# Kernel tuning notes

Measured on AMD Instinct MI355X. Metric: run time of the kernel, lower is better.

The kernel has to match this reference:

```python
import jax, jax.numpy as jnp
import numpy as np

B, H, S, D = 4, 16, 2048, 64
SCALE = 8.0  # sqrt(D)
NEG = -1000000000.0


def setup_inputs() -> dict:
    key = jax.random.key(0)
    kq, kk, kv = jax.random.split(key, 3)
    q = jax.random.normal(kq, (B, H, S, D), dtype=jnp.float32)
    k = jax.random.normal(kk, (B, H, S, D), dtype=jnp.float32)
    v = jax.random.normal(kv, (B, H, S, D), dtype=jnp.float32)
    # causal mask: True means masked out (matches torch masked_fill)
    mask = jnp.triu(jnp.ones((S, S), dtype=bool), k=1)[None, None, :, :]
    mask = jnp.broadcast_to(mask, (B, 1, S, S))
    return {"q": q, "k": k, "v": v, "mask": mask}


def reference(q, k, v, mask):
    # score = q @ k^T / scale  -> [B,H,S,S]
    score = jnp.einsum("bhqd,bhkd->bhqk", q, k) / SCALE
    score = jnp.where(mask, NEG, score)
    probs = jax.nn.softmax(score, axis=-1)
    context = jnp.einsum("bhqk,bhkd->bhqd", probs, v)
    return context
```

## Files before the change

kernel.cpp:

```cpp
#include <hip/hip_runtime.h>

#define SQ 2048
#define DH 64
#define BK 64
#define NQT 32
#define NBH 64
#define M0 8.0f

#define WS_BYTES ((size_t)2 * NBH * SQ * DH * 2)

typedef float f32x4 __attribute__((ext_vector_type(4)));
typedef __bf16 bf16x8 __attribute__((ext_vector_type(8)));
typedef _Float16 f16x4 __attribute__((ext_vector_type(4)));
typedef _Float16 f16x8 __attribute__((ext_vector_type(8)));
typedef __fp16 fp16x2 __attribute__((ext_vector_type(2)));
typedef unsigned short u16x8 __attribute__((ext_vector_type(8)));
typedef unsigned int u32x4 __attribute__((ext_vector_type(4)));

static __device__ __forceinline__ unsigned int pkbf(float a, float b) {
#if __has_builtin(__builtin_amdgcn_cvt_pk_bf16_f32)
  typedef __bf16 bf16x2 __attribute__((ext_vector_type(2)));
  bf16x2 r = __builtin_amdgcn_cvt_pk_bf16_f32(a, b);
  return __builtin_bit_cast(unsigned int, r);
#else
  unsigned int ua = __builtin_bit_cast(unsigned int, a);
  unsigned int ub = __builtin_bit_cast(unsigned int, b);
  ua += 0x7fffu + ((ua >> 16) & 1u);
  ub += 0x7fffu + ((ub >> 16) & 1u);
  return (ua >> 16) | (ub & 0xffff0000u);
#endif
}

static __device__ __forceinline__ unsigned int pkf16(float a, float b) {
  fp16x2 r = __builtin_amdgcn_cvt_pkrtz(a, b);
  return __builtin_bit_cast(unsigned int, r);
}

static __device__ __forceinline__ f32x4 mfma_qk(u16x8 a, u16x8 b, f32x4 c) {
  return __builtin_amdgcn_mfma_f32_16x16x32_bf16(
      __builtin_bit_cast(bf16x8, a), __builtin_bit_cast(bf16x8, b), c, 0, 0, 0);
}

static __device__ __forceinline__ f32x4 mfma_pv(f16x4 a, f16x4 b, f32x4 c) {
  return __builtin_amdgcn_mfma_f32_16x16x16f16(a, b, c, 0, 0, 0);
}

static __device__ __forceinline__ f32x4 mfma_pv32(f16x8 a, f16x8 b, f32x4 c) {
  return __builtin_amdgcn_mfma_f32_16x16x32_f16(a, b, c, 0, 0, 0);
}

static __device__ __forceinline__ void ld16(unsigned short* l, const unsigned short* g) {
  __builtin_amdgcn_global_load_lds(
      (const __attribute__((address_space(1))) unsigned int*)(const void*)g,
      (__attribute__((address_space(3))) unsigned int*)(void*)l, 16, 0, 0);
}

static __device__ __forceinline__ void store_tile(float* wb, float* dst,
                                                  const f32x4* o, int lane,
                                                  int l15, int quad) {
#pragma unroll
  for (int dt = 0; dt < 4; ++dt) {
    const int colw = dt * 16 + quad * 4;
    *(f32x4*)&wb[l15 * 64 + (colw ^ ((l15 & 3) * 16))] = o[dt];
  }
  __builtin_amdgcn_wave_barrier();
#pragma unroll
  for (int j = 0; j < 4; ++j) {
    const int row = j * 4 + (lane >> 4);
    const int colw = (lane & 15) * 4;
    f32x4 v = *(const f32x4*)&wb[row * 64 + (colw ^ ((row & 3) * 16))];
    *(f32x4*)&dst[row * 64 + colw] = v;
  }
}

__global__ __launch_bounds__(256) void prep(const float* __restrict__ K,
                                            const float* __restrict__ V,
                                            unsigned short* __restrict__ Kf,
                                            unsigned short* __restrict__ Vf) {
  const int bh = (int)blockIdx.x >> 5;
  const int st = (int)blockIdx.x & 31;
  const int tid = threadIdx.x;
  __shared__ __align__(16) unsigned short T[DH * 64];
  {
    const int kvb = (tid >> 4) * 4, vdb = (tid & 15) * 4;
    const float* vp = V + ((size_t)bh * SQ + st * 64 + kvb) * DH + vdb;
    f32x4 r0 = *(const f32x4*)vp, r1 = *(const f32x4*)(vp + DH),
          r2 = *(const f32x4*)(vp + 2 * DH), r3 = *(const f32x4*)(vp + 3 * DH);
    const int uu = kvb >> 3, h = (kvb >> 2) & 1;
#pragma unroll
    for (int i = 0; i < 4; ++i) {
      const int d = vdb + i;
      uint2 w = {pkf16(r0[i], r1[i]), pkf16(r2[i], r3[i])};
      *(uint2*)&T[d * 64 + ((uu ^ (d & 7)) * 8) + h * 4] = w;
    }
  }
  {
    const size_t kin = ((size_t)bh * SQ + st * 64) * DH;
    unsigned short* kfo = Kf + (size_t)bh * SQ * DH + (size_t)st * 64 * DH;
#pragma unroll
    for (int e = 0; e < 2; ++e) {
      const int L = tid * 2 + e;
      const int l15 = L & 15, quad = (L >> 4) & 3, c = (L >> 6) & 1, nt = (L >> 7) & 3;
      const int krow = (nt >> 1) * 32 + ((l15 >> 2) & 3) * 8 + (nt & 1) * 4 + (l15 & 3);
      const float* kp = K + kin + (size_t)krow * DH + (c * 4 + quad) * 8;
      f32x4 x = *(const f32x4*)kp, y = *(const f32x4*)(kp + 4);
      u32x4 w = {pkbf(x[0], x[1]), pkbf(x[2], x[3]), pkbf(y[0], y[1]), pkbf(y[2], y[3])};
      *(u32x4*)&kfo[L * 8] = w;
    }
  }
  __syncthreads();
  {
    unsigned short* vfo = Vf + (size_t)bh * SQ * DH + (size_t)st * 64 * DH;
#pragma unroll
    for (int e = 0; e < 2; ++e) {
      const int L = tid * 2 + e;
      const int l15 = L & 15, quad = (L >> 4) & 3, dt = (L >> 6) & 3, n2 = (L >> 8) & 1;
      const int d = dt * 16 + l15, uu = n2 * 4 + quad;
      u16x8 val = *(const u16x8*)&T[d * 64 + ((uu ^ (d & 7)) * 8)];
      *(u16x8*)&vfo[L * 8] = val;
    }
  }
}

__global__ __launch_bounds__(256, 4) void fa_main(
    const float* __restrict__ Q, const unsigned short* __restrict__ Kf,
    const unsigned short* __restrict__ Vf, float* __restrict__ O) {
  const int lin = (int)blockIdx.x;
  const int xcd = lin & 7, u = lin >> 3;
  const int hh = u & 7;
  const int pi = (int)((0x32104567BA98CDEFull >> ((u >> 3) * 4)) & 15u);
  const int bh = hh * 8 + xcd;
  const int tend = 2 * pi + 1;

  const int tid = threadIdx.x;
  const int wv = tid >> 6;
  const int lane = tid & 63;
  const int l15 = lane & 15;
  const int quad = lane >> 4;

  __shared__ __align__(16) unsigned short SS[2][BK * DH];

  const size_t hq = (size_t)bh * (SQ * DH);
  const unsigned short* KfH = Kf + (size_t)bh * SQ * DH;
  const unsigned short* VfH = Vf + (size_t)bh * SQ * DH;

  const int qbase = pi * 128 + wv * 32;
  const int dtw = 2 * pi + (wv >> 1);
  const int qo = (wv & 1) * 32;

  u16x8 qf[2][2];
  {
    const float scq = 0.125f * 1.4426950408889634f;
#pragma unroll
    for (int f = 0; f < 2; ++f) {
      const float* qp = Q + hq + (size_t)(qbase + 16 * f + l15) * DH + quad * 8;
#pragma unroll
      for (int c = 0; c < 2; ++c) {
        f32x4 x = *(const f32x4*)(qp + c * 32);
        f32x4 y = *(const f32x4*)(qp + c * 32 + 4);
        u32x4 w = {pkbf(x[0] * scq, x[1] * scq), pkbf(x[2] * scq, x[3] * scq),
                   pkbf(y[0] * scq, y[1] * scq), pkbf(y[2] * scq, y[3] * scq)};
        qf[f][c] = __builtin_bit_cast(u16x8, w);
      }
    }
  }

  f32x4 o0[4], o1[4], la0, la1;
#pragma unroll
  for (int dt = 0; dt < 4; ++dt) {
    o0[dt] = (f32x4){0.f, 0.f, 0.f, 0.f};
    o1[dt] = (f32x4){0.f, 0.f, 0.f, 0.f};
  }
  la0 = (f32x4){0.f, 0.f, 0.f, 0.f};
  la1 = (f32x4){0.f, 0.f, 0.f, 0.f};
  const f16x8 ones8 = {(_Float16)1.f, (_Float16)1.f, (_Float16)1.f, (_Float16)1.f,
                       (_Float16)1.f, (_Float16)1.f, (_Float16)1.f, (_Float16)1.f};

  auto stage = [&](unsigned short* W, int t) {
#pragma unroll
    for (int j = 0; j < 2; ++j) {
      const int off = wv * 1024 + j * 512 + lane * 8;
      ld16(&W[off], &KfH[(size_t)t * 4096 + off]);
    }
  };

  auto attend = [&](const unsigned short* Ks, int t, bool diag) {
    const unsigned short* vg = VfH + (size_t)t * 4096;
    f16x8 vb0[4];
#pragma unroll
    for (int dt = 0; dt < 4; ++dt)
      vb0[dt] = *(const f16x8*)&vg[(0 * 4 + dt) * 512 + lane * 8];
    f32x4 s0[4], s1[4];
#pragma unroll
    for (int nt = 0; nt < 4; ++nt) {
      f32x4 a0 = {-M0, -M0, -M0, -M0}, a1 = {-M0, -M0, -M0, -M0};
#pragma unroll
      for (int c = 0; c < 2; ++c) {
        u16x8 kf = *(const u16x8*)&Ks[(nt * 2 + c) * 512 + lane * 8];
        a0 = mfma_qk(kf, qf[0][c], a0);
        a1 = mfma_qk(kf, qf[1][c], a1);
      }
      s0[nt] = a0;
      s1[nt] = a1;
    }
    if (diag) {
#pragma unroll
      for (int nt = 0; nt < 4; ++nt)
#pragma unroll
        for (int r = 0; r < 4; ++r) {
          const int kvl = (nt >> 1) * 32 + quad * 8 + (nt & 1) * 4 + r;
          if (kvl > qo + l15) s0[nt][r] = -1e30f;
          if (kvl > qo + 16 + l15) s1[nt][r] = -1e30f;
        }
    }
    f16x8 pf0[2], pf1[2];
#pragma unroll
    for (int n2 = 0; n2 < 2; ++n2) {
      f32x4 pe0, po0, pe1, po1;
#pragma unroll
      for (int r = 0; r < 4; ++r) {
        pe0[r] = __builtin_amdgcn_exp2f(s0[2 * n2][r]);
        po0[r] = __builtin_amdgcn_exp2f(s0[2 * n2 + 1][r]);
        pe1[r] = __builtin_amdgcn_exp2f(s1[2 * n2][r]);
        po1[r] = __builtin_amdgcn_exp2f(s1[2 * n2 + 1][r]);
      }
      u32x4 w0 = {pkf16(pe0[0], pe0[1]), pkf16(pe0[2], pe0[3]),
                  pkf16(po0[0], po0[1]), pkf16(po0[2], po0[3])};
      u32x4 w1 = {pkf16(pe1[0], pe1[1]), pkf16(pe1[2], pe1[3]),
                  pkf16(po1[0], po1[1]), pkf16(po1[2], po1[3])};
      pf0[n2] = __builtin_bit_cast(f16x8, w0);
      pf1[n2] = __builtin_bit_cast(f16x8, w1);
    }
    f16x8 vb1[4];
#pragma unroll
    for (int dt = 0; dt < 4; ++dt)
      vb1[dt] = *(const f16x8*)&vg[(1 * 4 + dt) * 512 + lane * 8];
    la0 = mfma_pv32(ones8, pf0[0], la0);
    la1 = mfma_pv32(ones8, pf1[0], la1);
    la0 = mfma_pv32(ones8, pf0[1], la0);
    la1 = mfma_pv32(ones8, pf1[1], la1);
#pragma unroll
    for (int dt = 0; dt < 4; ++dt) {
      o0[dt] = mfma_pv32(vb0[dt], pf0[0], o0[dt]);
      o1[dt] = mfma_pv32(vb0[dt], pf1[0], o1[dt]);
    }
#pragma unroll
    for (int dt = 0; dt < 4; ++dt) {
      o0[dt] = mfma_pv32(vb1[dt], pf0[1], o0[dt]);
      o1[dt] = mfma_pv32(vb1[dt], pf1[1], o1[dt]);
    }
  };

  auto step = [&](int t, const unsigned short* R, unsigned short* W) {
    if (t <= dtw) attend(R, t, t == dtw);
    __syncthreads();
    if (t + 2 <= tend) stage(W, t + 2);
  };

  stage(SS[0], 0);
  __syncthreads();
  stage(SS[1], 1);
  for (int t = 0; t <= tend; t += 2) {
    step(t, SS[0], SS[0]);
    if (t + 1 <= tend) step(t + 1, SS[1], SS[1]);
  }

  float* wb = (float*)SS + wv * 1024;
  {
    const float inv = 1.0f / la0[0];
    f32x4 on[4];
#pragma unroll
    for (int dt = 0; dt < 4; ++dt) on[dt] = o0[dt] * inv;
    store_tile(wb, O + hq + (size_t)(qbase)*DH, on, lane, l15, quad);
  }
  {
    const float inv = 1.0f / la1[0];
    f32x4 on[4];
#pragma unroll
    for (int dt = 0; dt < 4; ++dt) on[dt] = o1[dt] * inv;
    store_tile(wb, O + hq + (size_t)(qbase + 16) * DH, on, lane, l15, quad);
  }
}

__global__ __launch_bounds__(256, 4) void fa_full(
    const float* __restrict__ Q, const float* __restrict__ K,
    const float* __restrict__ V, float* __restrict__ O) {
  const int lin = (int)blockIdx.x;
  const int xcd = lin & 7;
  const int u = lin >> 3;
  const int hh = u & 7;
  const int p = u >> 3;
  const int bh = hh * 8 + xcd;
  const int tid = threadIdx.x;
  const int wv = tid >> 6;
  const int lane = tid & 63;
  const int l15 = lane & 15;
  const int quad = lane >> 4;
  __shared__ __align__(16) unsigned short SMEM[2][2 * BK * DH];
  const size_t hbase = (size_t)bh * (SQ * DH);
  const int krr = tid >> 3, kcc = (tid & 7) * 8;
  const int kvb = (tid >> 4) * 4, vdb = (tid & 15) * 4;
#pragma unroll
  for (int ph = 0; ph < 2; ++ph) {
    const int qt = ph ? (NQT - 1 - p) : p;
    const int wq0 = qt * 64 + wv * 16;
    u16x8 qf[2];
    {
      const float scq = 0.125f * 1.4426950408889634f;
      const float* qp = Q + hbase + (size_t)(wq0 + l15) * DH + quad * 8;
#pragma unroll
      for (int c = 0; c < 2; ++c) {
        f32x4 x = *(const f32x4*)(qp + c * 32);
        f32x4 y = *(const f32x4*)(qp + c * 32 + 4);
        u32x4 w = {pkbf(x[0] * scq, x[1] * scq), pkbf(x[2] * scq, x[3] * scq),
                   pkbf(y[0] * scq, y[1] * scq), pkbf(y[2] * scq, y[3] * scq)};
        qf[c] = __builtin_bit_cast(u16x8, w);
      }
    }
    f32x4 o[4];
#pragma unroll
    for (int dt = 0; dt < 4; ++dt) o[dt] = (f32x4){0.f, 0.f, 0.f, 0.f};
    float l = 0.f;
    f32x4 ka[2][2], va[4];
    {
      const float* kp = K + hbase + (size_t)krr * DH + kcc;
      ka[0][0] = *(const f32x4*)kp;             ka[0][1] = *(const f32x4*)(kp + 4);
      ka[1][0] = *(const f32x4*)(kp + 32 * DH); ka[1][1] = *(const f32x4*)(kp + 32 * DH + 4);
      const float* vp = V + hbase + (size_t)kvb * DH + vdb;
      va[0] = *(const f32x4*)vp;            va[1] = *(const f32x4*)(vp + DH);
      va[2] = *(const f32x4*)(vp + 2 * DH); va[3] = *(const f32x4*)(vp + 3 * DH);
    }
    __syncthreads();
    {
      unsigned short* Ksn = SMEM[0];
      unsigned short* Vsn = SMEM[0] + BK * DH;
#pragma unroll
      for (int h = 0; h < 2; ++h) {
        const int rr = h * 32 + krr;
        u32x4 w = {pkbf(ka[h][0][0], ka[h][0][1]), pkbf(ka[h][0][2], ka[h][0][3]),
                   pkbf(ka[h][1][0], ka[h][1][1]), pkbf(ka[h][1][2], ka[h][1][3])};
        *(u32x4*)&Ksn[rr * DH + (kcc ^ ((rr & 7) * 8))] = w;
      }
#pragma unroll
      for (int i = 0; i < 4; ++i) {
        const int d = vdb + i;
        uint2 w = {pkf16(va[0][i], va[1][i]), pkf16(va[2][i], va[3][i])};
        *(uint2*)&Vsn[d * BK + (kvb ^ ((d & 15) * 4))] = w;
      }
    }
    __syncthreads();
    for (int t = 0; t <= qt; ++t) {
      const unsigned short* Ks = SMEM[t & 1];
      const unsigned short* Vs = SMEM[t & 1] + BK * DH;
      if (t < qt) {
        const int kb2 = (t + 1) * BK;
        const float* kp = K + hbase + (size_t)(kb2 + krr) * DH + kcc;
        ka[0][0] = *(const f32x4*)kp;             ka[0][1] = *(const f32x4*)(kp + 4);
        ka[1][0] = *(const f32x4*)(kp + 32 * DH); ka[1][1] = *(const f32x4*)(kp + 32 * DH + 4);
        const float* vp = V + hbase + (size_t)(kb2 + kvb) * DH + vdb;
        va[0] = *(const f32x4*)vp;            va[1] = *(const f32x4*)(vp + DH);
        va[2] = *(const f32x4*)(vp + 2 * DH); va[3] = *(const f32x4*)(vp + 3 * DH);
      }
      f32x4 s[4];
#pragma unroll
      for (int nt = 0; nt < 4; ++nt) {
        f32x4 acc = {-M0, -M0, -M0, -M0};
#pragma unroll
        for (int c = 0; c < 2; ++c) {
          const int row = nt * 16 + l15;
          u16x8 kf = *(const u16x8*)&Ks[row * DH + ((c * 32 + quad * 8) ^ ((l15 & 7) * 8))];
          acc = mfma_qk(kf, qf[c], acc);
        }
        s[nt] = acc;
      }
      if (t == qt) {
#pragma unroll
        for (int nt = 0; nt < 4; ++nt)
#pragma unroll
          for (int r = 0; r < 4; ++r)
            if (nt * 16 + quad * 4 + r > wv * 16 + l15) s[nt][r] = -1e30f;
      }
      f16x4 pf[4];
#pragma unroll
      for (int nt = 0; nt < 4; ++nt) {
        f32x4 pr;
#pragma unroll
        for (int r = 0; r < 4; ++r) { pr[r] = __builtin_amdgcn_exp2f(s[nt][r]); l += pr[r]; }
        uint2 w2 = {pkf16(pr[0], pr[1]), pkf16(pr[2], pr[3])};
        pf[nt] = __builtin_bit_cast(f16x4, w2);
      }
#pragma unroll
      for (int dt = 0; dt < 4; ++dt) {
        const int d = dt * 16 + l15;
#pragma unroll
        for (int nt = 0; nt < 4; ++nt) {
          f16x4 vf = *(const f16x4*)&Vs[d * BK + ((nt * 16 + quad * 4) ^ (l15 * 4))];
          o[dt] = mfma_pv(vf, pf[nt], o[dt]);
        }
      }
      if (t < qt) {
        unsigned short* Ksn = SMEM[(t + 1) & 1];
        unsigned short* Vsn = SMEM[(t + 1) & 1] + BK * DH;
#pragma unroll
        for (int h = 0; h < 2; ++h) {
          const int rr = h * 32 + krr;
          u32x4 w = {pkbf(ka[h][0][0], ka[h][0][1]), pkbf(ka[h][0][2], ka[h][0][3]),
                     pkbf(ka[h][1][0], ka[h][1][1]), pkbf(ka[h][1][2], ka[h][1][3])};
          *(u32x4*)&Ksn[rr * DH + (kcc ^ ((rr & 7) * 8))] = w;
        }
#pragma unroll
        for (int i = 0; i < 4; ++i) {
          const int d = vdb + i;
          uint2 w = {pkf16(va[0][i], va[1][i]), pkf16(va[2][i], va[3][i])};
          *(uint2*)&Vsn[d * BK + (kvb ^ ((d & 15) * 4))] = w;
        }
        __syncthreads();
      }
    }
    l += __shfl_xor(l, 16, 64);
    l += __shfl_xor(l, 32, 64);
    const float inv = 1.0f / l;
    f32x4 on[4];
#pragma unroll
    for (int dt = 0; dt < 4; ++dt) on[dt] = o[dt] * inv;
    float* wb = (float*)SMEM[(qt + 1) & 1] + wv * 1024;
    store_tile(wb, O + hbase + (size_t)wq0 * DH, on, lane, l15, quad);
  }
}

extern "C" void kernel_launch(void* const* d_in, const int* in_sizes, int n_in,
                              void* d_out, int out_size, void* d_ws, size_t ws_size,
                              hipStream_t stream) {
  const float* q = (const float*)d_in[0];
  const float* k = (const float*)d_in[1];
  const float* v = (const float*)d_in[2];
  float* o = (float*)d_out;
  if (ws_size >= WS_BYTES) {
    unsigned short* Kf = (unsigned short*)d_ws;
    unsigned short* Vf = Kf + (size_t)NBH * SQ * DH;
    prep<<<dim3(NBH * 32), 256, 0, stream>>>(k, v, Kf, Vf);
    fa_main<<<dim3(1024), 256, 0, stream>>>(q, Kf, Vf, o);
  } else {
    fa_full<<<dim3(1024), 256, 0, stream>>>(q, k, v, o);
  }
}
```

Before: 206.9 us.

## Stage K and V through a 4-deep LDS ring with 512-thread blocks

Doubles the block to 8 waves covering 256 query rows, so the grid drops to 512 blocks and each K/V tile is shared by more waves. K and V tiles are now both staged into LDS with async loads in a 4-slot ring buffer, three tiles ahead. Manual vmcnt waits and raw barriers replace __syncthreads. The aim is to hide global latency and cut redundant V reads from global memory. In exchange it uses far more LDS per block, which may limit occupancy, and the hand-tuned wait counts are fragile.

After: 204.0 us. No clear change (-1.4%).

```diff
diff --git a/kernel.cpp b/kernel.cpp
--- a/kernel.cpp
+++ b/kernel.cpp
@@ -16,6 +16,8 @@
 typedef __fp16 fp16x2 __attribute__((ext_vector_type(2)));
 typedef unsigned short u16x8 __attribute__((ext_vector_type(8)));
 typedef unsigned int u32x4 __attribute__((ext_vector_type(4)));
+
+#define WAIT_VM(N) asm volatile("s_waitcnt vmcnt(" #N ")" ::: "memory")
 
 static __device__ __forceinline__ unsigned int pkbf(float a, float b) {
 #if __has_builtin(__builtin_amdgcn_cvt_pk_bf16_f32)
@@ -122,15 +124,15 @@
   }
 }
 
-__global__ __launch_bounds__(256, 4) void fa_main(
+__global__ __launch_bounds__(512, 4) void fa_main(
     const float* __restrict__ Q, const unsigned short* __restrict__ Kf,
     const unsigned short* __restrict__ Vf, float* __restrict__ O) {
   const int lin = (int)blockIdx.x;
   const int xcd = lin & 7, u = lin >> 3;
   const int hh = u & 7;
-  const int pi = (int)((0x32104567BA98CDEFull >> ((u >> 3) * 4)) & 15u);
+  const int p = (int)((0x32104567u >> ((u >> 3) * 4)) & 15u);
   const int bh = hh * 8 + xcd;
-  const int tend = 2 * pi + 1;
+  const int tend = 4 * p + 3;
 
   const int tid = threadIdx.x;
   const int wv = tid >> 6;
@@ -138,14 +140,14 @@
   const int l15 = lane & 15;
   const int quad = lane >> 4;
 
-  __shared__ __align__(16) unsigned short SS[2][BK * DH];
+  __shared__ __align__(16) unsigned short SS[4][8192];
 
   const size_t hq = (size_t)bh * (SQ * DH);
   const unsigned short* KfH = Kf + (size_t)bh * SQ * DH;
   const unsigned short* VfH = Vf + (size_t)bh * SQ * DH;
 
-  const int qbase = pi * 128 + wv * 32;
-  const int dtw = 2 * pi + (wv >> 1);
+  const int qbase = p * 256 + wv * 32;
+  const int dtw = 4 * p + (wv >> 1);
   const int qo = (wv & 1) * 32;
 
   u16x8 qf[2][2];
@@ -180,16 +182,16 @@
 #pragma unroll
     for (int j = 0; j < 2; ++j) {
       const int off = wv * 1024 + j * 512 + lane * 8;
-      ld16(&W[off], &KfH[(size_t)t * 4096 + off]);
+      const unsigned short* src = (off < 4096)
+                                      ? &KfH[(size_t)t * 4096 + off]
+                                      : &VfH[(size_t)t * 4096 + (off - 4096)];
+      ld16(&W[off], src);
     }
   };
 
-  auto attend = [&](const unsigned short* Ks, int t, bool diag) {
-    const unsigned short* vg = VfH + (size_t)t * 4096;
-    f16x8 vb0[4];
-#pragma unroll
-    for (int dt = 0; dt < 4; ++dt)
-      vb0[dt] = *(const f16x8*)&vg[(0 * 4 + dt) * 512 + lane * 8];
+  auto attend = [&](const unsigned short* B, bool diag) {
+    const unsigned short* Ks = B;
+    const unsigned short* Vs = B + 4096;
     f32x4 s0[4], s1[4];
 #pragma unroll
     for (int nt = 0; nt < 4; ++nt) {
@@ -231,38 +233,42 @@
       pf0[n2] = __builtin_bit_cast(f16x8, w0);
       pf1[n2] = __builtin_bit_cast(f16x8, w1);
     }
-    f16x8 vb1[4];
-#pragma unroll
-    for (int dt = 0; dt < 4; ++dt)
-      vb1[dt] = *(const f16x8*)&vg[(1 * 4 + dt) * 512 + lane * 8];
-    la0 = mfma_pv32(ones8, pf0[0], la0);
-    la1 = mfma_pv32(ones8, pf1[0], la1);
-    la0 = mfma_pv32(ones8, pf0[1], la0);
-    la1 = mfma_pv32(ones8, pf1[1], la1);
+#pragma unroll
+    for (int n2 = 0; n2 < 2; ++n2) {
+      la0 = mfma_pv32(ones8, pf0[n2], la0);
+      la1 = mfma_pv32(ones8, pf1[n2], la1);
+    }
 #pragma unroll
     for (int dt = 0; dt < 4; ++dt) {
-      o0[dt] = mfma_pv32(vb0[dt], pf0[0], o0[dt]);
-      o1[dt] = mfma_pv32(vb0[dt], pf1[0], o1[dt]);
-    }
-#pragma unroll
-    for (int dt = 0; dt < 4; ++dt) {
-      o0[dt] = mfma_pv32(vb1[dt], pf0[1], o0[dt]);
-      o1[dt] = mfma_pv32(vb1[dt], pf1[1], o1[dt]);
+#pragma unroll
+      for (int n2 = 0; n2 < 2; ++n2) {
+        f16x8 vf = *(const f16x8*)&Vs[(n2 * 4 + dt) * 512 + lane * 8];
+        o0[dt] = mfma_pv32(vf, pf0[n2], o0[dt]);
+        o1[dt] = mfma_pv32(vf, pf1[n2], o1[dt]);
+      }
     }
   };
 
-  auto step = [&](int t, const unsigned short* R, unsigned short* W) {
-    if (t <= dtw) attend(R, t, t == dtw);
-    __syncthreads();
-    if (t + 2 <= tend) stage(W, t + 2);
-  };
-
   stage(SS[0], 0);
-  __syncthreads();
   stage(SS[1], 1);
-  for (int t = 0; t <= tend; t += 2) {
-    step(t, SS[0], SS[0]);
-    if (t + 1 <= tend) step(t + 1, SS[1], SS[1]);
+  stage(SS[2], 2);
+  WAIT_VM(4);
+  __builtin_amdgcn_s_barrier();
+  __builtin_amdgcn_sched_barrier(0);
+
+  for (int t = 0; t <= tend; ++t) {
+    if (t + 3 <= tend) stage(SS[(t + 3) & 3], t + 3);
+    if (t <= dtw) attend(SS[t & 3], t == dtw);
+    const int rem = tend - t;
+    if (rem >= 3) {
+      WAIT_VM(4);
+    } else if (rem == 2) {
+      WAIT_VM(2);
+    } else {
+      WAIT_VM(0);
+    }
+    __builtin_amdgcn_s_barrier();
+    __builtin_amdgcn_sched_barrier(0);
   }
 
   float* wb = (float*)SS + wv * 1024;
@@ -439,7 +445,7 @@
     unsigned short* Kf = (unsigned short*)d_ws;
     unsigned short* Vf = Kf + (size_t)NBH * SQ * DH;
     prep<<<dim3(NBH * 32), 256, 0, stream>>>(k, v, Kf, Vf);
-    fa_main<<<dim3(1024), 256, 0, stream>>>(q, Kf, Vf, o);
+    fa_main<<<dim3(512), 512, 0, stream>>>(q, Kf, Vf, o);
   } else {
     fa_full<<<dim3(1024), 256, 0, stream>>>(q, k, v, o);
   }
```
